# Performance work log

Measured on AMD Instinct MI355X. Metric: run time of the kernel, lower is better.

The kernel has to match this reference:

```python
import jax, jax.numpy as jnp
import numpy as np

N_EMBD = 1024
N_HEAD = 16
D_HEAD = N_EMBD // N_HEAD
B, T = 4, 2048


def _layernorm(x, g, b, eps=1e-5):
    mu = jnp.mean(x, axis=-1, keepdims=True)
    var = jnp.var(x, axis=-1, keepdims=True)
    return (x - mu) * jax.lax.rsqrt(var + eps) * g + b


def setup_inputs() -> dict:
    key = jax.random.key(0)
    ks = jax.random.split(key, 16)
    C = N_EMBD
    s = 0.02
    return {
        "x": jax.random.normal(ks[0], (B, T, C), jnp.float32),
        "ln1_g": jnp.ones((C,), jnp.float32),
        "ln1_b": jnp.zeros((C,), jnp.float32),
        "Wq": jax.random.normal(ks[1], (C, C), jnp.float32) * s,
        "bq": jnp.zeros((C,), jnp.float32),
        "Wk": jax.random.normal(ks[2], (C, C), jnp.float32) * s,
        "bk": jnp.zeros((C,), jnp.float32),
        "Wv": jax.random.normal(ks[3], (C, C), jnp.float32) * s,
        "bv": jnp.zeros((C,), jnp.float32),
        "Wo": jax.random.normal(ks[4], (C, C), jnp.float32) * s,
        "bo": jnp.zeros((C,), jnp.float32),
        "ln2_g": jnp.ones((C,), jnp.float32),
        "ln2_b": jnp.zeros((C,), jnp.float32),
        "W1": jax.random.normal(ks[5], (C, 4 * C), jnp.float32) * s,
        "b1": jnp.zeros((4 * C,), jnp.float32),
        "W2": jax.random.normal(ks[6], (4 * C, C), jnp.float32) * s,
        "b2": jnp.zeros((C,), jnp.float32),
    }


def reference(x, ln1_g, ln1_b, Wq, bq, Wk, bk, Wv, bv, Wo, bo,
              ln2_g, ln2_b, W1, b1, W2, b2):
    Bx, Tx, C = x.shape
    H, D = N_HEAD, D_HEAD

    # --- attention (pre-LN) ---
    h = _layernorm(x, ln1_g, ln1_b)
    q = (h @ Wq + bq).reshape(Bx, Tx, H, D)
    k = (h @ Wk + bk).reshape(Bx, Tx, H, D)
    v = (h @ Wv + bv).reshape(Bx, Tx, H, D)
    att = jnp.einsum("bqhd,bkhd->bhqk", q, k) * (1.0 / jnp.sqrt(jnp.float32(D)))
    causal = jnp.tril(jnp.ones((Tx, Tx), bool))
    att = jnp.where(causal, att, -jnp.inf)
    att = jax.nn.softmax(att, axis=-1)
    y = jnp.einsum("bhqk,bkhd->bqhd", att, v).reshape(Bx, Tx, C)
    x = x + (y @ Wo + bo)

    # --- MLP (pre-LN), exact GELU as in torch F.gelu default ---
    h2 = _layernorm(x, ln2_g, ln2_b)
    m = jax.nn.gelu(h2 @ W1 + b1, approximate=False)
    x = x + (m @ W2 + b2)
    return x
```

## Files before the change

kernel.cpp:

```cpp
#include <hip/hip_runtime.h>
#include <hip/hip_bf16.h>
#include <math.h>

#define C_EMBD 1024
#define T_SEQ  2048
#define BATCH  4
#define NHEAD  16
#define DHEAD  64

typedef __attribute__((ext_vector_type(8))) short bf16x8;
typedef __attribute__((ext_vector_type(4))) float floatx4;

#if __has_builtin(__builtin_amdgcn_exp2f)
#define EXP2F __builtin_amdgcn_exp2f
#else
#define EXP2F exp2f
#endif

static __device__ __forceinline__ floatx4 mfma16(bf16x8 a, bf16x8 b, floatx4 c) {
    return __builtin_amdgcn_mfma_f32_16x16x32_bf16(a, b, c, 0, 0, 0);
}

static __device__ __forceinline__ void gl2lds16(const void* g, void* l) {
    __builtin_amdgcn_global_load_lds(
        (const __attribute__((address_space(1))) void*)g,
        (__attribute__((address_space(3))) void*)l, 16, 0, 0);
}

__global__ __launch_bounds__(256) void transpose_cvt(
        const float* __restrict__ W, __hip_bfloat16* __restrict__ Wt, int K, int N) {
    __shared__ float tile[32][33];
    const int tid = threadIdx.x;
    const int n0 = blockIdx.x * 32, k0 = blockIdx.y * 32;
    const int r = tid >> 3, c4 = (tid & 7) * 4;
    float4 v = *(const float4*)&W[(size_t)(k0 + r) * N + n0 + c4];
    tile[r][c4 + 0] = v.x; tile[r][c4 + 1] = v.y;
    tile[r][c4 + 2] = v.z; tile[r][c4 + 3] = v.w;
    __syncthreads();
    __align__(8) __hip_bfloat16 ob[4];
    ob[0] = __float2bfloat16(tile[c4 + 0][r]);
    ob[1] = __float2bfloat16(tile[c4 + 1][r]);
    ob[2] = __float2bfloat16(tile[c4 + 2][r]);
    ob[3] = __float2bfloat16(tile[c4 + 3][r]);
    *(short4*)&Wt[(size_t)(n0 + r) * K + k0 + c4] = *(short4*)ob;
}

__global__ __launch_bounds__(256) void ln_bf16(
        const float* __restrict__ x, const float* __restrict__ g,
        const float* __restrict__ b, __hip_bfloat16* __restrict__ out) {
    const int row = blockIdx.x, tid = threadIdx.x;
    const float4 v = ((const float4*)(x + (size_t)row * C_EMBD))[tid];
    float s  = v.x + v.y + v.z + v.w;
    float sq = v.x * v.x + v.y * v.y + v.z * v.z + v.w * v.w;
    #pragma unroll
    for (int off = 1; off < 64; off <<= 1) {
        s  += __shfl_xor(s, off);
        sq += __shfl_xor(sq, off);
    }
    __shared__ float ps[4], pq[4];
    if ((tid & 63) == 0) { ps[tid >> 6] = s; pq[tid >> 6] = sq; }
    __syncthreads();
    s  = ps[0] + ps[1] + ps[2] + ps[3];
    sq = pq[0] + pq[1] + pq[2] + pq[3];
    const float mu   = s * (1.0f / C_EMBD);
    const float var  = sq * (1.0f / C_EMBD) - mu * mu;
    const float rstd = rsqrtf(var + 1e-5f);
    const float4 gv = ((const float4*)g)[tid];
    const float4 bv = ((const float4*)b)[tid];
    __align__(8) __hip_bfloat16 ob[4];
    ob[0] = __float2bfloat16((v.x - mu) * rstd * gv.x + bv.x);
    ob[1] = __float2bfloat16((v.y - mu) * rstd * gv.y + bv.y);
    ob[2] = __float2bfloat16((v.z - mu) * rstd * gv.z + bv.z);
    ob[3] = __float2bfloat16((v.w - mu) * rstd * gv.w + bv.w);
    *(short4*)&out[(size_t)row * C_EMBD + tid * 4] = *(short4*)ob;
}

template <int EP>
__global__ __launch_bounds__(256, 2) void gemm_bt(
        const __hip_bfloat16* __restrict__ A, const __hip_bfloat16* __restrict__ Bt,
        int M, int N, int K,
        const float* __restrict__ ba, const float* __restrict__ bb, const float* __restrict__ bc,
        __hip_bfloat16* __restrict__ o0, __hip_bfloat16* __restrict__ o1,
        __hip_bfloat16* __restrict__ o2, float* __restrict__ of,
        const float* __restrict__ resid) {
    __shared__ __align__(16) __hip_bfloat16 As[128 * 32];
    __shared__ __align__(16) __hip_bfloat16 Bs[128 * 32];
    const int tid  = threadIdx.x;
    const int n0   = blockIdx.x * 128;
    const int m0   = blockIdx.y * 128;
    const int wave = tid >> 6, lane = tid & 63;
    const int l15  = lane & 15, quad = lane >> 4;
    const int wm   = (wave & 1) * 64, wn = (wave >> 1) * 64;
    const int c0   = wave * 2;
    const int sr   = lane >> 2;
    const int sc   = (lane & 3) * 8;

    const floatx4 z4 = {0.f, 0.f, 0.f, 0.f};
    floatx4 acc[4][4];
    #pragma unroll
    for (int i = 0; i < 4; i++)
        #pragma unroll
        for (int j = 0; j < 4; j++) acc[i][j] = z4;

    for (int k0 = 0; k0 < K; k0 += 32) {
        __syncthreads();
        gl2lds16(&A[(m0 + c0 * 16 + sr) * K + k0 + sc],       &As[c0 * 512]);
        gl2lds16(&A[(m0 + (c0 + 1) * 16 + sr) * K + k0 + sc], &As[(c0 + 1) * 512]);
        gl2lds16(&Bt[(n0 + c0 * 16 + sr) * K + k0 + sc],      &Bs[c0 * 512]);
        gl2lds16(&Bt[(n0 + (c0 + 1) * 16 + sr) * K + k0 + sc],&Bs[(c0 + 1) * 512]);
        __syncthreads();
        bf16x8 af[4], bfr[4];
        #pragma unroll
        for (int i = 0; i < 4; i++)
            af[i] = *(const bf16x8*)&As[(wm + i * 16 + l15) * 32 + quad * 8];
        #pragma unroll
        for (int j = 0; j < 4; j++)
            bfr[j] = *(const bf16x8*)&Bs[(wn + j * 16 + l15) * 32 + quad * 8];
        #pragma unroll
        for (int i = 0; i < 4; i++)
            #pragma unroll
            for (int j = 0; j < 4; j++)
                acc[i][j] = mfma16(af[i], bfr[j], acc[i][j]);
    }

    #pragma unroll
    for (int i = 0; i < 4; i++) {
        #pragma unroll
        for (int j = 0; j < 4; j++) {
            const int col = n0 + wn + j * 16 + l15;
            #pragma unroll
            for (int r = 0; r < 4; r++) {
                const int m = m0 + wm + i * 16 + quad * 4 + r;
                float val = acc[i][j][r];
                if (EP == 0) {
                    const int which = col >> 10, cn = col & 1023;
                    const float* bp = (which == 0) ? ba : (which == 1) ? bb : bc;
                    val += bp[cn];
                    const int head = cn >> 6, d = cn & 63;
                    const int bidx = m >> 11, t = m & 2047;
                    if (which == 0) {
                        val *= 0.18033688011112042f;
                        o0[((bidx * NHEAD + head) * T_SEQ + t) * DHEAD + d] = __float2bfloat16(val);
                    } else if (which == 1) {
                        o1[((bidx * NHEAD + head) * T_SEQ + t) * DHEAD + d] = __float2bfloat16(val);
                    } else {
                        o2[((bidx * NHEAD + head) * DHEAD + d) * T_SEQ + t] = __float2bfloat16(val);
                    }
                } else if (EP == 1) {
                    val += ba[col];
                    of[m * N + col] = resid[m * N + col] + val;
                } else if (EP == 2) {
                    val += ba[col];
                    const float gl = 0.5f * val * (1.0f + erff(val * 0.70710678118654752f));
                    o0[m * N + col] = __float2bfloat16(gl);
                } else {
                    val += ba[col];
                    of[m * N + col] += val;
                }
            }
        }
    }
}

__global__ __launch_bounds__(256, 2) void attn_fa(
        const __hip_bfloat16* __restrict__ q, const __hip_bfloat16* __restrict__ k,
        const __hip_bfloat16* __restrict__ vt, __hip_bfloat16* __restrict__ y) {
    __shared__ __align__(16) __hip_bfloat16 Ks[2][64 * 64];
    __shared__ __align__(16) __hip_bfloat16 Vs[2][64 * 64];
    __shared__ __align__(16) __hip_bfloat16 pl[4][32 * 72];
    const int tid = threadIdx.x;
    const int wave = tid >> 6, lane = tid & 63;
    const int l15 = lane & 15, quad = lane >> 4;
    const int sw  = l15 & 7;
    const int lr  = lane >> 3;
    const int gsw = (lane & 7) ^ lr;

    const int lin  = blockIdx.x;
    const int xcd  = lin & 7;
    const int slot = lin >> 3;
    const int bh   = xcd * 8 + (slot >> 3);
    const int jA   = slot & 7;

    const __hip_bfloat16* qp = q + (size_t)bh * T_SEQ * DHEAD;
    const __hip_bfloat16* kp = k + (size_t)bh * T_SEQ * DHEAD;
    const __hip_bfloat16* vp = vt + (size_t)bh * DHEAD * T_SEQ;
    __hip_bfloat16* myp = &pl[wave][0];
    const int b = bh >> 4, head = bh & 15;
    const floatx4 z4 = {0.f, 0.f, 0.f, 0.f};

    auto stage = [&](const int buf, const int kb) {
        #pragma unroll
        for (int j = 0; j < 2; j++) {
            const int rb = wave * 16 + j * 8;
            gl2lds16(&kp[(size_t)(kb + rb + lr) * DHEAD + gsw * 8], &Ks[buf][rb * 64]);
            gl2lds16(&vp[(size_t)(rb + lr) * T_SEQ + kb + gsw * 8], &Vs[buf][rb * 64]);
        }
    };

    auto segment = [&](const int tile) {
        const int q0 = tile * 128;
        const int qw = q0 + wave * 32;
        const int cc = tile * 2 + 1;

        bf16x8 bq[2][2];
        #pragma unroll
        for (int qi = 0; qi < 2; qi++)
            #pragma unroll
            for (int h = 0; h < 2; h++)
                bq[qi][h] = *(const bf16x8*)&qp[(qw + qi * 16 + l15) * DHEAD + h * 32 + quad * 8];

        floatx4 oac[2][4];
        #pragma unroll
        for (int qi = 0; qi < 2; qi++)
            #pragma unroll
            for (int nd = 0; nd < 4; nd++) oac[qi][nd] = z4;
        float li[2] = {0.f, 0.f};

        stage(0, 0);

        for (int t = 0; t <= cc; t++) {
            const int cur = t & 1;
            if (t < cc) {
                stage(cur ^ 1, (t + 1) * 64);
                asm volatile("s_waitcnt vmcnt(4)" ::: "memory");
            } else {
                asm volatile("s_waitcnt vmcnt(0)" ::: "memory");
            }
            __builtin_amdgcn_s_barrier();
            asm volatile("" ::: "memory");

            const int kb = t * 64;
            const bool act = (kb <= qw + 31);
            if (act) {
                const bool dg = (kb + 63 > qw);
                bf16x8 kf[4][2];
                #pragma unroll
                for (int nt = 0; nt < 4; nt++)
                    #pragma unroll
                    for (int h = 0; h < 2; h++)
                        kf[nt][h] = *(const bf16x8*)&Ks[cur][(nt * 16 + l15) * 64 + (((h * 4 + quad) ^ sw) * 8)];
                floatx4 sa[2][4];
                #pragma unroll
                for (int qi = 0; qi < 2; qi++)
                    #pragma unroll
                    for (int nt = 0; nt < 4; nt++) sa[qi][nt] = z4;
                #pragma unroll
                for (int nt = 0; nt < 4; nt++)
                    #pragma unroll
                    for (int h = 0; h < 2; h++) {
                        sa[0][nt] = mfma16(kf[nt][h], bq[0][h], sa[0][nt]);
                        sa[1][nt] = mfma16(kf[nt][h], bq[1][h], sa[1][nt]);
                    }
                if (dg) {
                    #pragma unroll
                    for (int qi = 0; qi < 2; qi++)
                        #pragma unroll
                        for (int nt = 0; nt < 4; nt++)
                            #pragma unroll
                            for (int r = 0; r < 4; r++)
                                if (kb + nt * 16 + quad * 4 + r > qw + qi * 16 + l15)
                                    sa[qi][nt][r] = -INFINITY;
                }
                #pragma unroll
                for (int qi = 0; qi < 2; qi++) {
                    float sm = 0.f;
                    #pragma unroll
                    for (int nt = 0; nt < 4; nt++) {
                        __align__(8) __hip_bfloat16 pk[4];
                        #pragma unroll
                        for (int r = 0; r < 4; r++) {
                            const float p = EXP2F(sa[qi][nt][r]);
                            sm += p;
                            pk[r] = __float2bfloat16(p);
                        }
                        *(short4*)&myp[(qi * 16 + l15) * 72 + nt * 16 + quad * 4] = *(short4*)pk;
                    }
                    li[qi] += sm;
                }
                bf16x8 vf[4][2];
                #pragma unroll
                for (int nd = 0; nd < 4; nd++)
                    #pragma unroll
                    for (int kh = 0; kh < 2; kh++)
                        vf[nd][kh] = *(const bf16x8*)&Vs[cur][(nd * 16 + l15) * 64 + (((kh * 4 + quad) ^ sw) * 8)];
                asm volatile("s_waitcnt lgkmcnt(0)" ::: "memory");
                bf16x8 pf[2][2];
                #pragma unroll
                for (int qi = 0; qi < 2; qi++)
                    #pragma unroll
                    for (int kh = 0; kh < 2; kh++)
                        pf[qi][kh] = *(const bf16x8*)&myp[(qi * 16 + l15) * 72 + kh * 32 + quad * 8];
                #pragma unroll
                for (int nd = 0; nd < 4; nd++)
                    #pragma unroll
                    for (int kh = 0; kh < 2; kh++) {
                        oac[0][nd] = mfma16(vf[nd][kh], pf[0][kh], oac[0][nd]);
                        oac[1][nd] = mfma16(vf[nd][kh], pf[1][kh], oac[1][nd]);
                    }
            }
            asm volatile("" ::: "memory");
            __builtin_amdgcn_s_barrier();
        }

        float inv[2];
        #pragma unroll
        for (int qi = 0; qi < 2; qi++) {
            float l = li[qi];
            l += __shfl_xor(l, 16);
            l += __shfl_xor(l, 32);
            inv[qi] = 1.0f / l;
        }
        #pragma unroll
        for (int qi = 0; qi < 2; qi++)
            #pragma unroll
            for (int nd = 0; nd < 4; nd++) {
                __align__(8) __hip_bfloat16 ok[4];
                #pragma unroll
                for (int r = 0; r < 4; r++) ok[r] = __float2bfloat16(oac[qi][nd][r] * inv[qi]);
                *(short4*)&myp[(qi * 16 + l15) * 72 + nd * 16 + quad * 4] = *(short4*)ok;
            }
        asm volatile("s_waitcnt lgkmcnt(0)" ::: "memory");
        #pragma unroll
        for (int half = 0; half < 2; half++) {
            const int row = half * 16 + (lane >> 2);
            const int cb  = (lane & 3) * 16;
            const bf16x8 v0 = *(const bf16x8*)&myp[row * 72 + cb];
            const bf16x8 v1 = *(const bf16x8*)&myp[row * 72 + cb + 8];
            __hip_bfloat16* yr = &y[(size_t)(b * T_SEQ + qw + row) * C_EMBD + head * DHEAD + cb];
            *(bf16x8*)yr       = v0;
            *(bf16x8*)(yr + 8) = v1;
        }
        asm volatile("s_waitcnt vmcnt(0)" ::: "memory");
    };

    segment(jA);
    segment(15 - jA);
}

extern "C" void kernel_launch(void* const* d_in, const int* in_sizes, int n_in,
                              void* d_out, int out_size, void* d_ws, size_t ws_size,
                              hipStream_t stream) {
    const float* x     = (const float*)d_in[0];
    const float* ln1_g = (const float*)d_in[1];
    const float* ln1_b = (const float*)d_in[2];
    const float* Wq    = (const float*)d_in[3];
    const float* bq    = (const float*)d_in[4];
    const float* Wk    = (const float*)d_in[5];
    const float* bk    = (const float*)d_in[6];
    const float* Wv    = (const float*)d_in[7];
    const float* bv    = (const float*)d_in[8];
    const float* Wo    = (const float*)d_in[9];
    const float* bo    = (const float*)d_in[10];
    const float* ln2_g = (const float*)d_in[11];
    const float* ln2_b = (const float*)d_in[12];
    const float* W1    = (const float*)d_in[13];
    const float* b1    = (const float*)d_in[14];
    const float* W2    = (const float*)d_in[15];
    const float* b2    = (const float*)d_in[16];
    float* out = (float*)d_out;

    char* ws = (char*)d_ws;
    __hip_bfloat16* wqkvt = (__hip_bfloat16*)(ws);
    __hip_bfloat16* wot   = (__hip_bfloat16*)(ws + 6291456);
    __hip_bfloat16* w1t   = (__hip_bfloat16*)(ws + 8388608);
    __hip_bfloat16* w2t   = (__hip_bfloat16*)(ws + 16777216);
    __hip_bfloat16* hbuf  = (__hip_bfloat16*)(ws + 25165824);
    __hip_bfloat16* qbuf  = (__hip_bfloat16*)(ws + 41943040);
    __hip_bfloat16* kbuf  = (__hip_bfloat16*)(ws + 58720256);
    __hip_bfloat16* vbuf  = (__hip_bfloat16*)(ws + 75497472);
    __hip_bfloat16* ybuf  = (__hip_bfloat16*)(ws + 92274688);
    __hip_bfloat16* mbuf  = (__hip_bfloat16*)(ws + 41943040);

    transpose_cvt<<<dim3(32, 32), 256, 0, stream>>>(Wq, wqkvt, 1024, 1024);
    transpose_cvt<<<dim3(32, 32), 256, 0, stream>>>(Wk, wqkvt + 1024 * 1024, 1024, 1024);
    transpose_cvt<<<dim3(32, 32), 256, 0, stream>>>(Wv, wqkvt + 2048 * 1024, 1024, 1024);
    transpose_cvt<<<dim3(32, 32), 256, 0, stream>>>(Wo, wot, 1024, 1024);
    transpose_cvt<<<dim3(128, 32), 256, 0, stream>>>(W1, w1t, 1024, 4096);
    transpose_cvt<<<dim3(32, 128), 256, 0, stream>>>(W2, w2t, 4096, 1024);

    ln_bf16<<<8192, 256, 0, stream>>>(x, ln1_g, ln1_b, hbuf);

    gemm_bt<0><<<dim3(24, 64), 256, 0, stream>>>(hbuf, wqkvt, 8192, 3072, 1024,
        bq, bk, bv, qbuf, kbuf, vbuf, nullptr, nullptr);

    attn_fa<<<dim3(512), 256, 0, stream>>>(qbuf, kbuf, vbuf, ybuf);

    gemm_bt<1><<<dim3(8, 64), 256, 0, stream>>>(ybuf, wot, 8192, 1024, 1024,
        bo, nullptr, nullptr, nullptr, nullptr, nullptr, out, x);

    ln_bf16<<<8192, 256, 0, stream>>>(out, ln2_g, ln2_b, hbuf);

    gemm_bt<2><<<dim3(32, 64), 256, 0, stream>>>(hbuf, w1t, 8192, 4096, 1024,
        b1, nullptr, nullptr, mbuf, nullptr, nullptr, nullptr, nullptr);

    gemm_bt<3><<<dim3(8, 64), 256, 0, stream>>>(mbuf, w2t, 8192, 1024, 4096,
        b2, nullptr, nullptr, nullptr, nullptr, nullptr, out, nullptr);
}
```

Baseline: 551.8 us.

## Double-buffer GEMM LDS tiles and remap workgroups for XCD/L2 locality

Splits the GEMM shared-memory tiles into two buffers so the global-to-LDS load of the next K slice is issued before the MFMAs on the current slice. This replaces the two barriers per iteration with one manual waitcnt plus barrier. It also remaps the linear block index so consecutive blocks on the same XCD cover nearby output tiles, aiming for better L2 reuse. LDS use doubles, which may reduce occupancy, and the remap assumes the grid size is a multiple of 8.

```diff
diff --git a/kernel.cpp b/kernel.cpp
--- a/kernel.cpp
+++ b/kernel.cpp
@@ -83,11 +83,20 @@
         __hip_bfloat16* __restrict__ o0, __hip_bfloat16* __restrict__ o1,
         __hip_bfloat16* __restrict__ o2, float* __restrict__ of,
         const float* __restrict__ resid) {
-    __shared__ __align__(16) __hip_bfloat16 As[128 * 32];
-    __shared__ __align__(16) __hip_bfloat16 Bs[128 * 32];
+    __shared__ __align__(16) __hip_bfloat16 As[2][128 * 32];
+    __shared__ __align__(16) __hip_bfloat16 Bs[2][128 * 32];
     const int tid  = threadIdx.x;
-    const int n0   = blockIdx.x * 128;
-    const int m0   = blockIdx.y * 128;
+
+    const int gx  = gridDim.x;
+    const int nwg = gx * gridDim.y;
+    const int lin = blockIdx.x + gx * blockIdx.y;
+    const int cpx = nwg >> 3;
+    const int wg  = (lin & 7) * cpx + (lin >> 3);
+    const int by  = (wg & 7) + 8 * (wg / (gx << 3));
+    const int bx  = (wg >> 3) % gx;
+    const int n0  = bx * 128;
+    const int m0  = by * 128;
+
     const int wave = tid >> 6, lane = tid & 63;
     const int l15  = lane & 15, quad = lane >> 4;
     const int wm   = (wave & 1) * 64, wn = (wave >> 1) * 64;
@@ -102,25 +111,38 @@
         #pragma unroll
         for (int j = 0; j < 4; j++) acc[i][j] = z4;
 
-    for (int k0 = 0; k0 < K; k0 += 32) {
-        __syncthreads();
-        gl2lds16(&A[(m0 + c0 * 16 + sr) * K + k0 + sc],       &As[c0 * 512]);
-        gl2lds16(&A[(m0 + (c0 + 1) * 16 + sr) * K + k0 + sc], &As[(c0 + 1) * 512]);
-        gl2lds16(&Bt[(n0 + c0 * 16 + sr) * K + k0 + sc],      &Bs[c0 * 512]);
-        gl2lds16(&Bt[(n0 + (c0 + 1) * 16 + sr) * K + k0 + sc],&Bs[(c0 + 1) * 512]);
-        __syncthreads();
+    auto stage = [&](const int buf, const int k0) {
+        gl2lds16(&A [(m0 + c0 * 16 + sr) * K + k0 + sc],       &As[buf][c0 * 512]);
+        gl2lds16(&A [(m0 + (c0 + 1) * 16 + sr) * K + k0 + sc], &As[buf][(c0 + 1) * 512]);
+        gl2lds16(&Bt[(n0 + c0 * 16 + sr) * K + k0 + sc],       &Bs[buf][c0 * 512]);
+        gl2lds16(&Bt[(n0 + (c0 + 1) * 16 + sr) * K + k0 + sc], &Bs[buf][(c0 + 1) * 512]);
+    };
+
+    stage(0, 0);
+    asm volatile("s_waitcnt vmcnt(0)" ::: "memory");
+    __builtin_amdgcn_s_barrier();
+    asm volatile("" ::: "memory");
+
+    const int nk = K >> 5;
+    int cur = 0;
+    for (int t = 0; t < nk; ++t) {
+        if (t + 1 < nk) stage(cur ^ 1, (t + 1) * 32);
         bf16x8 af[4], bfr[4];
         #pragma unroll
         for (int i = 0; i < 4; i++)
-            af[i] = *(const bf16x8*)&As[(wm + i * 16 + l15) * 32 + quad * 8];
+            af[i] = *(const bf16x8*)&As[cur][(wm + i * 16 + l15) * 32 + quad * 8];
         #pragma unroll
         for (int j = 0; j < 4; j++)
-            bfr[j] = *(const bf16x8*)&Bs[(wn + j * 16 + l15) * 32 + quad * 8];
+            bfr[j] = *(const bf16x8*)&Bs[cur][(wn + j * 16 + l15) * 32 + quad * 8];
         #pragma unroll
         for (int i = 0; i < 4; i++)
             #pragma unroll
             for (int j = 0; j < 4; j++)
                 acc[i][j] = mfma16(af[i], bfr[j], acc[i][j]);
+        asm volatile("s_waitcnt lgkmcnt(0) vmcnt(0)" ::: "memory");
+        __builtin_amdgcn_s_barrier();
+        asm volatile("" ::: "memory");
+        cur ^= 1;
     }
 
     #pragma unroll
```

After: 549.6 us. No clear change (-0.4%).
